# Optimization experiments

Measured on AMD Instinct MI355X. Metric: run time of the kernel, lower is better.

The kernel has to match this reference:

```python
import jax, jax.numpy as jnp
import numpy as np

N, E = 50000, 800000
IN, H, C = 256, 8, 32  # heads=8, hidden_dim=32 -> out dim 256
NEG_SLOPE = 0.2
EPS = 1e-5


def setup_inputs() -> dict:
    key = jax.random.key(0)
    ks = jax.random.split(key, 6)
    x = jax.random.normal(ks[0], (N, IN), jnp.float32)
    edge_index = jax.random.randint(ks[1], (2, E), 0, N, dtype=jnp.int32)
    W = jax.random.normal(ks[2], (IN, H * C), jnp.float32) / np.sqrt(IN).astype(np.float32)
    att_src = jax.random.normal(ks[3], (H, C), jnp.float32) * 0.1
    att_dst = jax.random.normal(ks[4], (H, C), jnp.float32) * 0.1
    bias = jnp.zeros((H * C,), jnp.float32)
    gamma = jnp.ones((H * C,), jnp.float32)
    beta = jnp.zeros((H * C,), jnp.float32)
    return {"x": x, "edge_index": edge_index, "W": W, "att_src": att_src,
            "att_dst": att_dst, "bias": bias, "gamma": gamma, "beta": beta}


def reference(x, edge_index, W, att_src, att_dst, bias, gamma, beta):
    n = x.shape[0]
    # Linear projection -> per-head features [N, H, C]
    xl = (x @ W).reshape(n, H, C)
    # Per-node attention half-logits [N, H]
    a_src = jnp.einsum('nhc,hc->nh', xl, att_src)
    a_dst = jnp.einsum('nhc,hc->nh', xl, att_dst)
    # Add self loops (PyG GATConv default)
    loops = jnp.arange(n, dtype=edge_index.dtype)
    src = jnp.concatenate([edge_index[0], loops])  # [E+N]
    dst = jnp.concatenate([edge_index[1], loops])
    # Edge attention logits + segment softmax over destination neighborhoods
    logits = jax.nn.leaky_relu(a_src[src] + a_dst[dst], NEG_SLOPE)  # [E+N, H]
    seg_max = jax.ops.segment_max(logits, dst, num_segments=n)
    ex = jnp.exp(logits - seg_max[dst])
    denom = jax.ops.segment_sum(ex, dst, num_segments=n)
    alpha = ex / denom[dst]  # [E+N, H]
    # Weighted scatter-aggregation of source features
    msgs = xl[src] * alpha[:, :, None]  # [E+N, H, C]
    out = jax.ops.segment_sum(msgs, dst, num_segments=n).reshape(n, H * C) + bias
    # LayerNorm over feature dim
    mu = jnp.mean(out, axis=-1, keepdims=True)
    var = jnp.var(out, axis=-1, keepdims=True)
    return (out - mu) / jnp.sqrt(var + EPS) * gamma + beta
```

## Files before the change

### kernel.cpp

```cpp
#include <hip/hip_runtime.h>
#include <math.h>

#define NEG 0.2f
#define LNEPS 1e-5f

typedef __attribute__((ext_vector_type(8))) short bf16x8;
typedef __attribute__((ext_vector_type(8))) unsigned short u16x8;
typedef __attribute__((ext_vector_type(4))) float f32x4;

__device__ __forceinline__ float lrelu(float x){ return x > 0.f ? x : NEG*x; }

__device__ __forceinline__ short f2b(float f){
  unsigned u = __float_as_uint(f);
  unsigned r = u + 0x7fffu + ((u >> 16) & 1u);
  return (short)(r >> 16);
}
__device__ __forceinline__ float b2f(unsigned short u){
  return __uint_as_float(((unsigned)u) << 16);
}

__global__ __launch_bounds__(256) void wt_k(const float* __restrict__ W,
                                            unsigned short* __restrict__ WT){
  int idx = blockIdx.x*256 + threadIdx.x;
  int k = idx >> 8, c = idx & 255;
  WT[c*256 + k] = (unsigned short)f2b(W[idx]);
}

__device__ __forceinline__ void load_half(float4 nx[8], const float* p){
  #pragma unroll
  for (int s=0;s<4;s++){
    nx[2*s]   = *(const float4*)(p + s*32);
    nx[2*s+1] = *(const float4*)(p + s*32 + 4);
  }
}
__device__ __forceinline__ void cvt_half(bf16x8 af[4], const float4 nx[8]){
  #pragma unroll
  for (int s=0;s<4;s++){
    af[s][0]=f2b(nx[2*s].x);   af[s][1]=f2b(nx[2*s].y);
    af[s][2]=f2b(nx[2*s].z);   af[s][3]=f2b(nx[2*s].w);
    af[s][4]=f2b(nx[2*s+1].x); af[s][5]=f2b(nx[2*s+1].y);
    af[s][6]=f2b(nx[2*s+1].z); af[s][7]=f2b(nx[2*s+1].w);
  }
}

__global__ __launch_bounds__(256, 2) void mfma_gemm_k(const float* __restrict__ A,
    const unsigned short* __restrict__ WT, unsigned short* __restrict__ Cb,
    const float* __restrict__ att_src, const float* __restrict__ att_dst,
    float* __restrict__ a_src, float* __restrict__ a_dst, int M, int nTiles){
  int w   = threadIdx.x >> 6;
  int l   = threadIdx.x & 63;
  int l15 = l & 15;
  int kg  = l >> 4;
  int colbase = w*64;

  bf16x8 bfr[4][8];
  #pragma unroll
  for (int j=0;j<4;j++){
    const unsigned short* bp = WT + (size_t)(colbase + j*16 + l15)*256 + kg*8;
    #pragma unroll
    for (int ks=0;ks<8;ks++) bfr[j][ks] = *(const bf16x8*)(bp + ks*32);
  }
  float as_r[4], ad_r[4];
  #pragma unroll
  for (int j=0;j<4;j++){
    as_r[j] = att_src[colbase + j*16 + l15];
    ad_r[j] = att_dst[colbase + j*16 + l15];
  }

  int t = blockIdx.x;
  if (t >= nTiles) return;
  int row0 = t*16 + l15;
  const float* ap = A + (size_t)(row0 < M ? row0 : M-1)*256 + kg*8;
  float4 nx[8];
  load_half(nx, ap);

  while (t < nTiles){
    f32x4 acc[4];
    #pragma unroll
    for (int j=0;j<4;j++) acc[j] = (f32x4){0.f,0.f,0.f,0.f};
    bf16x8 af[4];

    cvt_half(af, nx);
    load_half(nx, ap + 128);
    #pragma unroll
    for (int s=0;s<4;s++)
      #pragma unroll
      for (int j=0;j<4;j++)
        acc[j] = __builtin_amdgcn_mfma_f32_16x16x32_bf16(af[s], bfr[j][s], acc[j], 0, 0, 0);

    int tn = t + gridDim.x;
    int rown = tn < nTiles ? tn*16 + l15 : row0;
    const float* apn = A + (size_t)(rown < M ? rown : M-1)*256 + kg*8;

    cvt_half(af, nx);
    load_half(nx, apn);
    #pragma unroll
    for (int s=0;s<4;s++)
      #pragma unroll
      for (int j=0;j<4;j++)
        acc[j] = __builtin_amdgcn_mfma_f32_16x16x32_bf16(af[s], bfr[j][4+s], acc[j], 0, 0, 0);

    int orow_base = t*16 + kg*4;
    #pragma unroll
    for (int j=0;j<4;j++)
      #pragma unroll
      for (int rr=0;rr<4;rr++){
        int orow = orow_base + rr;
        if (orow < M) Cb[(size_t)orow*256 + colbase + j*16 + l15] = (unsigned short)f2b(acc[j][rr]);
      }
    #pragma unroll
    for (int rr=0;rr<4;rr++){
      float p0s = acc[0][rr]*as_r[0] + acc[1][rr]*as_r[1];
      float p0d = acc[0][rr]*ad_r[0] + acc[1][rr]*ad_r[1];
      float p1s = acc[2][rr]*as_r[2] + acc[3][rr]*as_r[3];
      float p1d = acc[2][rr]*ad_r[2] + acc[3][rr]*ad_r[3];
      #pragma unroll
      for (int m=1;m<16;m<<=1){
        p0s += __shfl_xor(p0s,m); p0d += __shfl_xor(p0d,m);
        p1s += __shfl_xor(p1s,m); p1d += __shfl_xor(p1d,m);
      }
      int orow = orow_base + rr;
      if (l15==0 && orow < M){
        a_src[(size_t)orow*8 + 2*w]   = p0s;
        a_dst[(size_t)orow*8 + 2*w]   = p0d;
        a_src[(size_t)orow*8 + 2*w+1] = p1s;
        a_dst[(size_t)orow*8 + 2*w+1] = p1d;
      }
    }
    t = tn; row0 = rown; ap = apn;
  }
}

__global__ void dinit_k(int* __restrict__ deg, int n){
  int i = blockIdx.x*blockDim.x+threadIdx.x;
  if (i<n) deg[i]=1;
}

__global__ void deg_k(const int* __restrict__ dst, int* __restrict__ deg, int E){
  int e = blockIdx.x*blockDim.x+threadIdx.x;
  if (e<E) atomicAdd(&deg[dst[e]],1);
}

__global__ __launch_bounds__(1024) void scan1_k(const int* __restrict__ deg,
                                                int* __restrict__ off,
                                                int* __restrict__ bsum, int n){
  __shared__ int wsum[16];
  int tid=threadIdx.x, lane=tid&63, wid=tid>>6;
  int i = blockIdx.x*1024 + tid;
  int v = (i<n)?deg[i]:0;
  int x = v;
  #pragma unroll
  for (int s=1;s<64;s<<=1){ int t2=__shfl_up(x,s); if (lane>=s) x+=t2; }
  if (lane==63) wsum[wid]=x;
  __syncthreads();
  if (tid<16){
    int y=wsum[tid];
    #pragma unroll
    for (int s=1;s<16;s<<=1){ int t2=__shfl_up(y,s); if (tid>=s) y+=t2; }
    wsum[tid]=y;
  }
  __syncthreads();
  int prefix=(wid? wsum[wid-1]:0);
  if (i<n) off[i]=prefix + x - v;
  if (tid==0) bsum[blockIdx.x]=wsum[15];
}

__global__ void scan2_k(int* __restrict__ bsum, int nb, int* __restrict__ offn){
  int lane = threadIdx.x;
  int v = (lane<nb)?bsum[lane]:0;
  int x = v;
  #pragma unroll
  for (int s=1;s<64;s<<=1){ int t2=__shfl_up(x,s); if (lane>=s) x+=t2; }
  if (lane<nb) bsum[lane] = x - v;
  if (lane==63) *offn = x;
}

__global__ __launch_bounds__(1024) void scan3_k(int* __restrict__ off,
                                                const int* __restrict__ bsum, int n){
  int i = blockIdx.x*1024 + threadIdx.x;
  if (i<n) off[i] += bsum[blockIdx.x];
}

__global__ void self_k(const int* __restrict__ off, int* __restrict__ sorted,
                       int* __restrict__ cur, int n){
  int i = blockIdx.x*blockDim.x+threadIdx.x;
  if (i<n){ sorted[off[i]] = i; cur[i] = 1; }
}

__global__ void scatter_k(const int* __restrict__ src, const int* __restrict__ dst,
                          const int* __restrict__ off, int* __restrict__ cur,
                          int* __restrict__ sorted, int E){
  int e=blockIdx.x*blockDim.x+threadIdx.x;
  if (e<E){
    int d=dst[e];
    int pos=off[d]+atomicAdd(&cur[d],1);
    sorted[pos]=src[e];
  }
}

__global__ __launch_bounds__(256) void agg3_k(const unsigned short* __restrict__ xlb,
    const float* __restrict__ a_src, const float* __restrict__ a_dst,
    const int* __restrict__ off, const int* __restrict__ sorted,
    const float* __restrict__ bias, const float* __restrict__ gamma,
    const float* __restrict__ beta, float* __restrict__ out, int n){
  int node = blockIdx.x*4 + (threadIdx.x>>6);
  if (node >= n) return;
  int lane = threadIdx.x & 63;
  int half = lane >> 5;
  int sl   = lane & 31;
  int h    = sl >> 2;
  float adst = a_dst[(size_t)node*8 + h];
  int s0 = off[node], dd = off[node+1] - s0;

  float acc[8] = {0.f,0.f,0.f,0.f,0.f,0.f,0.f,0.f};
  float den = 0.f;

  int i = 0;
  for (; i+8 <= dd; i += 8){
    int s[4];
    #pragma unroll
    for (int j=0;j<4;j++) s[j] = sorted[s0 + i + 2*j + half];
    u16x8 u[4];
    #pragma unroll
    for (int j=0;j<4;j++) u[j] = *(const u16x8*)(xlb + (size_t)s[j]*256 + sl*8);
    float wv[4];
    #pragma unroll
    for (int j=0;j<4;j++) wv[j] = __expf(lrelu(a_src[(size_t)s[j]*8+h]+adst));
    #pragma unroll
    for (int j=0;j<4;j++){
      den += wv[j];
      #pragma unroll
      for (int k=0;k<8;k++) acc[k] += wv[j]*b2f((unsigned short)u[j][k]);
    }
  }
  for (; i < dd; i += 2){
    int idx = i + half;
    bool ok = idx < dd;
    int s1 = ok ? sorted[s0+idx] : node;
    u16x8 u1 = *(const u16x8*)(xlb + (size_t)s1*256 + sl*8);
    float w1 = ok ? __expf(lrelu(a_src[(size_t)s1*8+h]+adst)) : 0.f;
    den += w1;
    #pragma unroll
    for (int k=0;k<8;k++) acc[k] += w1*b2f((unsigned short)u1[k]);
  }

  den += __shfl_xor(den, 32);
  #pragma unroll
  for (int k=0;k<8;k++) acc[k] += __shfl_xor(acc[k], 32);

  float rd = 1.0f/den;
  float4 bia0 = *(const float4*)(bias + sl*8);
  float4 bia1 = *(const float4*)(bias + sl*8 + 4);
  float o[8];
  o[0]=acc[0]*rd+bia0.x; o[1]=acc[1]*rd+bia0.y; o[2]=acc[2]*rd+bia0.z; o[3]=acc[3]*rd+bia0.w;
  o[4]=acc[4]*rd+bia1.x; o[5]=acc[5]*rd+bia1.y; o[6]=acc[6]*rd+bia1.z; o[7]=acc[7]*rd+bia1.w;

  float sum=0.f, ssq=0.f;
  #pragma unroll
  for (int k=0;k<8;k++){ sum += o[k]; ssq += o[k]*o[k]; }
  #pragma unroll
  for (int s=1;s<32;s<<=1){ sum += __shfl_xor(sum,s); ssq += __shfl_xor(ssq,s); }
  float mean = sum*(1.0f/256.0f);
  float var  = ssq*(1.0f/256.0f) - mean*mean;
  float rstd = rsqrtf(var + LNEPS);

  int f = sl*8 + half*4;
  float4 g  = *(const float4*)(gamma + f);
  float4 be = *(const float4*)(beta + f);
  int kb = half*4;
  float4 ov;
  ov.x = (o[kb+0]-mean)*rstd*g.x+be.x;
  ov.y = (o[kb+1]-mean)*rstd*g.y+be.y;
  ov.z = (o[kb+2]-mean)*rstd*g.z+be.z;
  ov.w = (o[kb+3]-mean)*rstd*g.w+be.w;
  *(float4*)(out + (size_t)node*256 + f) = ov;
}

extern "C" void kernel_launch(void* const* d_in, const int* in_sizes, int n_in,
                              void* d_out, int out_size, void* d_ws, size_t ws_size,
                              hipStream_t stream){
  const float* x       = (const float*)d_in[0];
  const int*   ei      = (const int*)  d_in[1];
  const float* W       = (const float*)d_in[2];
  const float* att_src = (const float*)d_in[3];
  const float* att_dst = (const float*)d_in[4];
  const float* bias    = (const float*)d_in[5];
  const float* gamma   = (const float*)d_in[6];
  const float* beta    = (const float*)d_in[7];
  float* out = (float*)d_out;

  int N = in_sizes[0]/256;
  int E = in_sizes[1]/2;
  const int* srcp = ei;
  const int* dstp = ei + E;

  unsigned short* xlb = (unsigned short*)d_ws;
  float* a_src = (float*)(xlb + (size_t)N*256);
  float* a_dst = a_src + (size_t)N*8;
  int*   deg   = (int*)(a_dst + (size_t)N*8);
  int*   off   = deg + N;
  int*   cur   = off + N + 1;
  int*   sorted= cur + N;
  int*   bsum  = sorted + E + N;
  unsigned short* WT = (unsigned short*)(bsum + 1024);

  int nb = (N + 1023)/1024;
  int nTiles = (N + 15)/16;

  wt_k<<<256, 256, 0, stream>>>(W, WT);
  mfma_gemm_k<<<512, 256, 0, stream>>>(x, WT, xlb, att_src, att_dst, a_src, a_dst, N, nTiles);
  dinit_k<<<(N+255)/256, 256, 0, stream>>>(deg, N);
  deg_k<<<(E+255)/256, 256, 0, stream>>>(dstp, deg, E);
  scan1_k<<<nb, 1024, 0, stream>>>(deg, off, bsum, N);
  scan2_k<<<1, 64, 0, stream>>>(bsum, nb, off + N);
  scan3_k<<<nb, 1024, 0, stream>>>(off, bsum, N);
  self_k<<<(N+255)/256, 256, 0, stream>>>(off, sorted, cur, N);
  scatter_k<<<(E+255)/256, 256, 0, stream>>>(srcp, dstp, off, cur, sorted, E);
  agg3_k<<<(N+3)/4, 256, 0, stream>>>(xlb, a_src, a_dst, off, sorted, bias, gamma, beta, out, N);
}
```

Measured before the change: 209.7 us.

## Fold attention vectors into weights, fuse scan kernels, dedupe edge exp in aggregation

Precomputes W·att_src and W·att_dst as an extra 16-column bf16 weight block, so the GEMM produces the attention half-logits with one additional MFMA chain in wave 0 instead of a shuffle reduction over the accumulators. Merges the scan-add and self-loop kernels into one launch, and raises GEMM occupancy (launch bounds 4, grid 1024). In aggregation, each lane computes one (edge, head) exp and shares it by shuffle, removing the redundant per-lane exp and a_src loads. The logits now come from bf16-rounded projected weights, which changes numerics slightly, and the larger occupancy may pressure registers.

```diff
diff --git a/kernel.cpp b/kernel.cpp
--- a/kernel.cpp
+++ b/kernel.cpp
@@ -20,10 +20,27 @@
 }
 
 __global__ __launch_bounds__(256) void wt_k(const float* __restrict__ W,
-                                            unsigned short* __restrict__ WT){
-  int idx = blockIdx.x*256 + threadIdx.x;
-  int k = idx >> 8, c = idx & 255;
-  WT[c*256 + k] = (unsigned short)f2b(W[idx]);
+                                            const float* __restrict__ att_src,
+                                            const float* __restrict__ att_dst,
+                                            unsigned short* __restrict__ WT,
+                                            unsigned short* __restrict__ WS){
+  int b = blockIdx.x;
+  if (b < 256){
+    int idx = b*256 + threadIdx.x;
+    int k = idx >> 8, c = idx & 255;
+    WT[c*256 + k] = (unsigned short)f2b(W[idx]);
+  } else {
+    int idx = (b-256)*256 + threadIdx.x;
+    int col = idx >> 8;
+    int k   = idx & 255;
+    int head = col & 7;
+    const float* av = (col < 8 ? att_src : att_dst) + head*32;
+    const float* wr = W + (size_t)k*256 + head*32;
+    float sum = 0.f;
+    #pragma unroll
+    for (int c=0;c<32;c++) sum += wr[c]*av[c];
+    WS[col*256 + k] = (unsigned short)f2b(sum);
+  }
 }
 
 __device__ __forceinline__ void load_half(float4 nx[8], const float* p){
@@ -43,9 +60,9 @@
   }
 }
 
-__global__ __launch_bounds__(256, 2) void mfma_gemm_k(const float* __restrict__ A,
-    const unsigned short* __restrict__ WT, unsigned short* __restrict__ Cb,
-    const float* __restrict__ att_src, const float* __restrict__ att_dst,
+__global__ __launch_bounds__(256, 4) void mfma_gemm_k(const float* __restrict__ A,
+    const unsigned short* __restrict__ WT, const unsigned short* __restrict__ WS,
+    unsigned short* __restrict__ Cb,
     float* __restrict__ a_src, float* __restrict__ a_dst, int M, int nTiles){
   int w   = threadIdx.x >> 6;
   int l   = threadIdx.x & 63;
@@ -60,11 +77,11 @@
     #pragma unroll
     for (int ks=0;ks<8;ks++) bfr[j][ks] = *(const bf16x8*)(bp + ks*32);
   }
-  float as_r[4], ad_r[4];
-  #pragma unroll
-  for (int j=0;j<4;j++){
-    as_r[j] = att_src[colbase + j*16 + l15];
-    ad_r[j] = att_dst[colbase + j*16 + l15];
+  bf16x8 bfa[8];
+  if (w==0){
+    const unsigned short* bp = WS + (size_t)l15*256 + kg*8;
+    #pragma unroll
+    for (int ks=0;ks<8;ks++) bfa[ks] = *(const bf16x8*)(bp + ks*32);
   }
 
   int t = blockIdx.x;
@@ -78,15 +95,19 @@
     f32x4 acc[4];
     #pragma unroll
     for (int j=0;j<4;j++) acc[j] = (f32x4){0.f,0.f,0.f,0.f};
+    f32x4 acc_a = (f32x4){0.f,0.f,0.f,0.f};
     bf16x8 af[4];
 
     cvt_half(af, nx);
     load_half(nx, ap + 128);
     #pragma unroll
-    for (int s=0;s<4;s++)
+    for (int s=0;s<4;s++){
       #pragma unroll
       for (int j=0;j<4;j++)
         acc[j] = __builtin_amdgcn_mfma_f32_16x16x32_bf16(af[s], bfr[j][s], acc[j], 0, 0, 0);
+      if (w==0)
+        acc_a = __builtin_amdgcn_mfma_f32_16x16x32_bf16(af[s], bfa[s], acc_a, 0, 0, 0);
+    }
 
     int tn = t + gridDim.x;
     int rown = tn < nTiles ? tn*16 + l15 : row0;
@@ -95,10 +116,13 @@
     cvt_half(af, nx);
     load_half(nx, apn);
     #pragma unroll
-    for (int s=0;s<4;s++)
+    for (int s=0;s<4;s++){
       #pragma unroll
       for (int j=0;j<4;j++)
         acc[j] = __builtin_amdgcn_mfma_f32_16x16x32_bf16(af[s], bfr[j][4+s], acc[j], 0, 0, 0);
+      if (w==0)
+        acc_a = __builtin_amdgcn_mfma_f32_16x16x32_bf16(af[s], bfa[4+s], acc_a, 0, 0, 0);
+    }
 
     int orow_base = t*16 + kg*4;
     #pragma unroll
@@ -108,23 +132,14 @@
         int orow = orow_base + rr;
         if (orow < M) Cb[(size_t)orow*256 + colbase + j*16 + l15] = (unsigned short)f2b(acc[j][rr]);
       }
-    #pragma unroll
-    for (int rr=0;rr<4;rr++){
-      float p0s = acc[0][rr]*as_r[0] + acc[1][rr]*as_r[1];
-      float p0d = acc[0][rr]*ad_r[0] + acc[1][rr]*ad_r[1];
-      float p1s = acc[2][rr]*as_r[2] + acc[3][rr]*as_r[3];
-      float p1d = acc[2][rr]*ad_r[2] + acc[3][rr]*ad_r[3];
-      #pragma unroll
-      for (int m=1;m<16;m<<=1){
-        p0s += __shfl_xor(p0s,m); p0d += __shfl_xor(p0d,m);
-        p1s += __shfl_xor(p1s,m); p1d += __shfl_xor(p1d,m);
-      }
-      int orow = orow_base + rr;
-      if (l15==0 && orow < M){
-        a_src[(size_t)orow*8 + 2*w]   = p0s;
-        a_dst[(size_t)orow*8 + 2*w]   = p0d;
-        a_src[(size_t)orow*8 + 2*w+1] = p1s;
-        a_dst[(size_t)orow*8 + 2*w+1] = p1d;
+    if (w==0){
+      #pragma unroll
+      for (int rr=0;rr<4;rr++){
+        int orow = orow_base + rr;
+        if (orow < M){
+          if (l15 < 8) a_src[(size_t)orow*8 + l15]     = acc_a[rr];
+          else         a_dst[(size_t)orow*8 + l15 - 8] = acc_a[rr];
+        }
       }
     }
     t = tn; row0 = rown; ap = apn;
@@ -175,16 +190,14 @@
   if (lane==63) *offn = x;
 }
 
-__global__ __launch_bounds__(1024) void scan3_k(int* __restrict__ off,
-                                                const int* __restrict__ bsum, int n){
+__global__ __launch_bounds__(1024) void scan3self_k(int* __restrict__ off,
+    const int* __restrict__ bsum, int* __restrict__ sorted, int* __restrict__ cur, int n){
   int i = blockIdx.x*1024 + threadIdx.x;
-  if (i<n) off[i] += bsum[blockIdx.x];
-}
-
-__global__ void self_k(const int* __restrict__ off, int* __restrict__ sorted,
-                       int* __restrict__ cur, int n){
-  int i = blockIdx.x*blockDim.x+threadIdx.x;
-  if (i<n){ sorted[off[i]] = i; cur[i] = 1; }
+  if (i>=n) return;
+  int o = off[i] + bsum[blockIdx.x];
+  off[i] = o;
+  sorted[o] = i;
+  cur[i] = 1;
 }
 
 __global__ void scatter_k(const int* __restrict__ src, const int* __restrict__ dst,
@@ -198,7 +211,7 @@
   }
 }
 
-__global__ __launch_bounds__(256) void agg3_k(const unsigned short* __restrict__ xlb,
+__global__ __launch_bounds__(256) void agg5_k(const unsigned short* __restrict__ xlb,
     const float* __restrict__ a_src, const float* __restrict__ a_dst,
     const int* __restrict__ off, const int* __restrict__ sorted,
     const float* __restrict__ bias, const float* __restrict__ gamma,
@@ -209,7 +222,10 @@
   int half = lane >> 5;
   int sl   = lane & 31;
   int h    = sl >> 2;
-  float adst = a_dst[(size_t)node*8 + h];
+  int hh   = lane & 7;
+  int je   = lane >> 3;
+  float adst_h = a_dst[(size_t)node*8 + h];
+  float adst_e = a_dst[(size_t)node*8 + hh];
   int s0 = off[node], dd = off[node+1] - s0;
 
   float acc[8] = {0.f,0.f,0.f,0.f,0.f,0.f,0.f,0.f};
@@ -220,12 +236,14 @@
     int s[4];
     #pragma unroll
     for (int j=0;j<4;j++) s[j] = sorted[s0 + i + 2*j + half];
+    int se = sorted[s0 + i + je];
+    float w_l = __expf(lrelu(a_src[(size_t)se*8 + hh] + adst_e));
+    float wv[4];
+    #pragma unroll
+    for (int j=0;j<4;j++) wv[j] = __shfl(w_l, ((2*j+half)<<3) | h);
     u16x8 u[4];
     #pragma unroll
     for (int j=0;j<4;j++) u[j] = *(const u16x8*)(xlb + (size_t)s[j]*256 + sl*8);
-    float wv[4];
-    #pragma unroll
-    for (int j=0;j<4;j++) wv[j] = __expf(lrelu(a_src[(size_t)s[j]*8+h]+adst));
     #pragma unroll
     for (int j=0;j<4;j++){
       den += wv[j];
@@ -237,8 +255,8 @@
     int idx = i + half;
     bool ok = idx < dd;
     int s1 = ok ? sorted[s0+idx] : node;
+    float w1 = ok ? __expf(lrelu(a_src[(size_t)s1*8+h]+adst_h)) : 0.f;
     u16x8 u1 = *(const u16x8*)(xlb + (size_t)s1*256 + sl*8);
-    float w1 = ok ? __expf(lrelu(a_src[(size_t)s1*8+h]+adst)) : 0.f;
     den += w1;
     #pragma unroll
     for (int k=0;k<8;k++) acc[k] += w1*b2f((unsigned short)u1[k]);
@@ -303,18 +321,18 @@
   int*   sorted= cur + N;
   int*   bsum  = sorted + E + N;
   unsigned short* WT = (unsigned short*)(bsum + 1024);
+  unsigned short* WS = WT + 65536;
 
   int nb = (N + 1023)/1024;
   int nTiles = (N + 15)/16;
 
-  wt_k<<<256, 256, 0, stream>>>(W, WT);
-  mfma_gemm_k<<<512, 256, 0, stream>>>(x, WT, xlb, att_src, att_dst, a_src, a_dst, N, nTiles);
+  wt_k<<<272, 256, 0, stream>>>(W, att_src, att_dst, WT, WS);
+  mfma_gemm_k<<<1024, 256, 0, stream>>>(x, WT, WS, xlb, a_src, a_dst, N, nTiles);
   dinit_k<<<(N+255)/256, 256, 0, stream>>>(deg, N);
   deg_k<<<(E+255)/256, 256, 0, stream>>>(dstp, deg, E);
   scan1_k<<<nb, 1024, 0, stream>>>(deg, off, bsum, N);
   scan2_k<<<1, 64, 0, stream>>>(bsum, nb, off + N);
-  scan3_k<<<nb, 1024, 0, stream>>>(off, bsum, N);
-  self_k<<<(N+255)/256, 256, 0, stream>>>(off, sorted, cur, N);
+  scan3self_k<<<nb, 1024, 0, stream>>>(off, bsum, sorted, cur, N);
   scatter_k<<<(E+255)/256, 256, 0, stream>>>(srcp, dstp, off, cur, sorted, E);
-  agg3_k<<<(N+3)/4, 256, 0, stream>>>(xlb, a_src, a_dst, off, sorted, bias, gamma, beta, out, N);
-}
+  agg5_k<<<(N+3)/4, 256, 0, stream>>>(xlb, a_src, a_dst, off, sorted, bias, gamma, beta, out, N);
+}
```

New measurement: 286.6 us. +36.7%, slower.
